# Optimization experiments

Measured on AMD Instinct MI355X. Metric: run time of the kernel, lower is better.

The kernel has to match this reference:

```python
import jax, jax.numpy as jnp
import numpy as np

# Layer configuration (from init_kwargs)
T = 32
TSEQ = jnp.linspace(1.0 / T, 1.0, T, dtype=jnp.float32)  # tseq grid
N_HOM_DIMS = 2      # dimensions = [0, 1]
KMAX = 4            # KK = [0,1,2,3] -> top-4 landscapes

B, N, P = 128, 256 * 256, 4096  # batch, grid cells, persistence pairs


def setup_inputs() -> dict:
    key = jax.random.key(0)
    k1, k2, k3, k4 = jax.random.split(key, 4)
    fun_value = jax.random.uniform(k1, (B, N), dtype=jnp.float32)
    birth_idx = jax.random.randint(k2, (B, P), 0, N, dtype=jnp.int32)
    death_idx = jax.random.randint(k3, (B, P), 0, N, dtype=jnp.int32)
    pair_dim = jax.random.randint(k4, (B, P), 0, N_HOM_DIMS, dtype=jnp.int32)
    return {"fun_value": fun_value, "birth_idx": birth_idx,
            "death_idx": death_idx, "pair_dim": pair_dim}


def reference(fun_value, birth_idx, death_idx, pair_dim):
    # Gather birth/death filtration values of each persistence pair
    # (this is fun_value[locationBirth] / fun_value[locationDeath]).
    b = jnp.take_along_axis(fun_value, birth_idx, axis=-1)   # [B, P]
    d = jnp.take_along_axis(fun_value, death_idx, axis=-1)   # [B, P]
    # Tent functions: fab[b, t, p] = max(min(tseq[t] - birth_p, death_p - tseq[t]), 0)
    fab = jnp.maximum(
        jnp.minimum(TSEQ[None, :, None] - b[:, None, :],
                    d[:, None, :] - TSEQ[None, :, None]),
        0.0)                                                  # [B, T, P]
    # Restrict pairs to each homology dimension; out-of-dim pairs become the
    # zero padding the original code uses in its fab buffer.
    dims = jnp.arange(N_HOM_DIMS, dtype=pair_dim.dtype)
    in_dim = pair_dim[:, None, None, :] == dims[None, :, None, None]  # [B, D, 1, P]
    fab_d = jnp.where(in_dim, fab[:, None, :, :], 0.0)        # [B, D, T, P]
    # Landscape = top-KMAX values over pairs (== -sort(-fab)[..., KK]).
    land, _ = jax.lax.top_k(fab_d, KMAX)                      # [B, D, T, KMAX]
    return land
```

## Files before the change

### kernel.cpp

```cpp
#include <hip/hip_runtime.h>

#define B_ 128
#define N_ 65536
#define P_ 4096
#define T_ 32
#define D_ 2
#define K_ 4
#define S_ 8
#define PPB 512

#define INS(v0, v1, v2, v3, val)                                  \
    {                                                             \
        float _x = fminf(v0, val); v0 = fmaxf(v0, val);           \
        float _y = fminf(v1, _x);  v1 = fmaxf(v1, _x);            \
        float _z = fminf(v2, _y);  v2 = fmaxf(v2, _y);            \
        v3 = fmaxf(v3, _z);                                       \
    }

__global__ __launch_bounds__(256) void fused_scan(
        const float* __restrict__ fun,
        const int* __restrict__ bidx,
        const int* __restrict__ didx,
        const int* __restrict__ pdim,
        float* __restrict__ partial) {
    __shared__ float2 bdS[PPB + 8];
    __shared__ int    cntS[8];
    __shared__ float  mrg[4][64][4];

    int bid   = blockIdx.x;
    int xcd   = bid & 7;
    int seq   = bid >> 3;
    int batch = xcd * 16 + (seq & 15);
    int slice = seq >> 4;

    int tid  = threadIdx.x;
    int lane = tid & 63;
    int wave = tid >> 6;
    int base = batch * P_ + slice * PPB;

    const float* f = fun + (size_t)batch * N_;
    int p0 = base + tid, p1 = base + 256 + tid;
    int pd0 = pdim[p0], pd1 = pdim[p1];
    float b0 = f[bidx[p0]], d0 = f[didx[p0]];
    float b1 = f[bidx[p1]], d1 = f[didx[p1]];

    unsigned long long bal0 = __ballot(pd0 == 0);
    unsigned long long bal1 = __ballot(pd1 == 0);
    if (lane == 0) {
        cntS[wave * 2]     = __popcll(bal0);
        cntS[wave * 2 + 1] = __popcll(bal1);
    }
    __syncthreads();

    int s0 = wave * 2, s1 = s0 + 1;
    int pre0_s0 = 0, pre1_s0 = 0, pre0_s1 = 0, pre1_s1 = 0, n0tot = 0;
    #pragma unroll
    for (int s = 0; s < 8; ++s) {
        int cs = cntS[s];
        if (s < s0) { pre0_s0 += cs; pre1_s0 += 64 - cs; }
        if (s < s1) { pre0_s1 += cs; pre1_s1 += 64 - cs; }
        n0tot += cs;
    }
    int n1tot = PPB - n0tot;
    int A   = (n0tot + 1) & ~1;
    int n1p = (n1tot + 1) & ~1;

    unsigned long long lmask = (1ull << lane) - 1ull;
    int r0 = __popcll(bal0 & lmask);
    int r1 = __popcll(bal1 & lmask);
    int dst0 = (pd0 == 0) ? (pre0_s0 + r0) : (A + pre1_s0 + (lane - r0));
    int dst1 = (pd1 == 0) ? (pre0_s1 + r1) : (A + pre1_s1 + (lane - r1));
    bdS[dst0] = make_float2(b0, d0);
    bdS[dst1] = make_float2(b1, d1);
    if (tid == 0 && (n0tot & 1)) bdS[n0tot]     = make_float2(4.f, -4.f);
    if (tid == 1 && (n1tot & 1)) bdS[A + n1tot] = make_float2(4.f, -4.f);
    __syncthreads();

    int half = lane >> 5;
    int t    = lane & 31;
    float tf = (float)(t + 1) * 0.03125f;

    float a0 = 0.f, a1 = 0.f, a2 = 0.f, a3 = 0.f;
    float c0 = 0.f, c1 = 0.f, c2 = 0.f, c3 = 0.f;

    #pragma unroll 4
    for (int j = wave * 2; j < A; j += 8) {
        float2 p = bdS[j + half];
        float val = fminf(tf - p.x, p.y - tf);
        INS(a0, a1, a2, a3, val);
    }
    #pragma unroll 4
    for (int j = A + wave * 2; j < A + n1p; j += 8) {
        float2 p = bdS[j + half];
        float val = fminf(tf - p.x, p.y - tf);
        INS(c0, c1, c2, c3, val);
    }

    float u0 = (half == 0) ? a0 : c0, w0 = (half == 0) ? c0 : a0;
    float u1 = (half == 0) ? a1 : c1, w1 = (half == 0) ? c1 : a1;
    float u2 = (half == 0) ? a2 : c2, w2 = (half == 0) ? c2 : a2;
    float u3 = (half == 0) ? a3 : c3, w3 = (half == 0) ? c3 : a3;
    float q;
    q = __shfl_xor(w0, 32); INS(u0, u1, u2, u3, q);
    q = __shfl_xor(w1, 32); INS(u0, u1, u2, u3, q);
    q = __shfl_xor(w2, 32); INS(u0, u1, u2, u3, q);
    q = __shfl_xor(w3, 32); INS(u0, u1, u2, u3, q);

    mrg[wave][lane][0] = u0;
    mrg[wave][lane][1] = u1;
    mrg[wave][lane][2] = u2;
    mrg[wave][lane][3] = u3;
    __syncthreads();

    if (wave == 0) {
        float v0 = 0.f, v1 = 0.f, v2 = 0.f, v3 = 0.f;
        #pragma unroll
        for (int w = 0; w < 4; ++w) {
            #pragma unroll
            for (int k = 0; k < 4; ++k) {
                float val = mrg[w][lane][k];
                INS(v0, v1, v2, v3, val);
            }
        }
        float* dst = partial + (((size_t)batch * S_ + slice) * 64 + lane) * 4;
        dst[0] = v0; dst[1] = v1; dst[2] = v2; dst[3] = v3;
    }
}

__global__ __launch_bounds__(256) void final_merge(
        const float* __restrict__ partial,
        float* __restrict__ out) {
    int tid   = blockIdx.x * 256 + threadIdx.x;
    int batch = tid >> 6;
    int combo = tid & 63;
    float v0 = 0.f, v1 = 0.f, v2 = 0.f, v3 = 0.f;
    for (int s = 0; s < S_; ++s) {
        const float* src = partial + (((size_t)batch * S_ + s) * 64 + combo) * 4;
        #pragma unroll
        for (int k = 0; k < 4; ++k) {
            float val = src[k];
            INS(v0, v1, v2, v3, val);
        }
    }
    float* dst = out + (size_t)tid * 4;
    dst[0] = v0; dst[1] = v1; dst[2] = v2; dst[3] = v3;
}

extern "C" void kernel_launch(void* const* d_in, const int* in_sizes, int n_in,
                              void* d_out, int out_size, void* d_ws, size_t ws_size,
                              hipStream_t stream) {
    const float* fun  = (const float*)d_in[0];
    const int*   bidx = (const int*)d_in[1];
    const int*   didx = (const int*)d_in[2];
    const int*   pdim = (const int*)d_in[3];
    float* out = (float*)d_out;

    float* partial = (float*)d_ws;

    fused_scan<<<B_ * S_, 256, 0, stream>>>(fun, bidx, didx, pdim, partial);
    final_merge<<<(B_ * 64) / 256, 256, 0, stream>>>(partial, out);
}
```

Baseline: 89.61 us.

## Prefetch function rows via global_load_lds and vectorize index and partial loads

```diff
diff --git a/kernel.cpp b/kernel.cpp
--- a/kernel.cpp
+++ b/kernel.cpp
@@ -38,11 +38,30 @@
     int wave = tid >> 6;
     int base = batch * P_ + slice * PPB;
 
+    const int2* b2 = (const int2*)(bidx + base);
+    const int2* d2 = (const int2*)(didx + base);
+    const int2* p2 = (const int2*)(pdim + base);
+    int2 bi = b2[tid];
+    int2 di = d2[tid];
+    int2 pd = p2[tid];
+
+    {
+        const float* chunk = fun + (size_t)batch * N_ + slice * 8192
+                           + wave * 2048 + lane * 4;
+        char* ldsdst = (char*)&mrg[wave][0][0];
+        #pragma unroll
+        for (int k = 0; k < 8; ++k) {
+            __builtin_amdgcn_global_load_lds(
+                (const __attribute__((address_space(1))) unsigned int*)(chunk + k * 256),
+                (__attribute__((address_space(3))) unsigned int*)ldsdst,
+                16, 0, 0);
+        }
+    }
+
     const float* f = fun + (size_t)batch * N_;
-    int p0 = base + tid, p1 = base + 256 + tid;
-    int pd0 = pdim[p0], pd1 = pdim[p1];
-    float b0 = f[bidx[p0]], d0 = f[didx[p0]];
-    float b1 = f[bidx[p1]], d1 = f[didx[p1]];
+    float b0 = f[bi.x], d0 = f[di.x];
+    float b1 = f[bi.y], d1 = f[di.y];
+    int pd0 = pd.x, pd1 = pd.y;
 
     unsigned long long bal0 = __ballot(pd0 == 0);
     unsigned long long bal1 = __ballot(pd1 == 0);
@@ -85,14 +104,14 @@
 
     #pragma unroll 4
     for (int j = wave * 2; j < A; j += 8) {
-        float2 p = bdS[j + half];
-        float val = fminf(tf - p.x, p.y - tf);
+        float2 pr = bdS[j + half];
+        float val = fminf(tf - pr.x, pr.y - tf);
         INS(a0, a1, a2, a3, val);
     }
     #pragma unroll 4
     for (int j = A + wave * 2; j < A + n1p; j += 8) {
-        float2 p = bdS[j + half];
-        float val = fminf(tf - p.x, p.y - tf);
+        float2 pr = bdS[j + half];
+        float val = fminf(tf - pr.x, pr.y - tf);
         INS(c0, c1, c2, c3, val);
     }
 
@@ -122,8 +141,8 @@
                 INS(v0, v1, v2, v3, val);
             }
         }
-        float* dst = partial + (((size_t)batch * S_ + slice) * 64 + lane) * 4;
-        dst[0] = v0; dst[1] = v1; dst[2] = v2; dst[3] = v3;
+        float4* dstp = (float4*)(partial + (((size_t)batch * S_ + slice) * 64 + lane) * 4);
+        *dstp = make_float4(v0, v1, v2, v3);
     }
 }
 
@@ -134,16 +153,16 @@
     int batch = tid >> 6;
     int combo = tid & 63;
     float v0 = 0.f, v1 = 0.f, v2 = 0.f, v3 = 0.f;
+    const float4* src = (const float4*)(partial + ((size_t)batch * S_ * 64 + combo) * 4);
+    #pragma unroll
     for (int s = 0; s < S_; ++s) {
-        const float* src = partial + (((size_t)batch * S_ + s) * 64 + combo) * 4;
-        #pragma unroll
-        for (int k = 0; k < 4; ++k) {
-            float val = src[k];
-            INS(v0, v1, v2, v3, val);
-        }
+        float4 val4 = src[(size_t)s * 64];
+        INS(v0, v1, v2, v3, val4.x);
+        INS(v0, v1, v2, v3, val4.y);
+        INS(v0, v1, v2, v3, val4.z);
+        INS(v0, v1, v2, v3, val4.w);
     }
-    float* dst = out + (size_t)tid * 4;
-    dst[0] = v0; dst[1] = v1; dst[2] = v2; dst[3] = v3;
+    *(float4*)(out + (size_t)tid * 4) = make_float4(v0, v1, v2, v3);
 }
 
 extern "C" void kernel_launch(void* const* d_in, const int* in_sizes, int n_in,
```

After: 91.65 us. +2.3%, slower.
